# Performance work log

Hardware: AMD Instinct MI355X
Metric: run time of the kernel (lower is better)

The kernel has to match this reference:

```python
import jax, jax.numpy as jnp
import numpy as np

N = 50000      # total nodes across batched graphs
E = 400000     # directed edges (before self-loops)
B = 256        # number of graphs / protein embeddings
F_IN = 78      # atom features (num_features_xd)
H1, F1 = 10, 78   # gcn1: heads=10, out=78 -> concat 780
F2 = 128       # gcn2 output_dim (heads=1)
EMB = 320      # PLM embed_dim
PLM = 128      # plm_layers[0]
BN_EPS = 1e-5


def setup_inputs() -> dict:
    key = jax.random.key(0)
    ks = jax.random.split(key, 30)
    g = lambda k, s, sc=0.05: (jax.random.normal(k, s, jnp.float32) * sc)
    inp = {
        'x': jax.random.normal(ks[0], (N, F_IN), jnp.float32),
        'edge_index': jax.random.randint(ks[1], (2, E), 0, N),
        # deterministic sorted assignment guarantees every graph id in [0,B) is populated
        'batch': (jnp.arange(N) * B) // N,
        'target_embedding': jax.random.normal(ks[2], (B, EMB), jnp.float32),
        # GATConv 1 (78 -> 78, heads=10, concat)
        'W1': g(ks[3], (F_IN, H1 * F1)), 'a1s': g(ks[4], (H1, F1)), 'a1d': g(ks[5], (H1, F1)), 'b1': g(ks[6], (H1 * F1,)),
        # GATConv 2 (780 -> 128, heads=1)
        'W2': g(ks[7], (H1 * F1, F2)), 'a2s': g(ks[8], (1, F2)), 'a2d': g(ks[9], (1, F2)), 'b2': g(ks[10], (F2,)),
        # fc_g1
        'Wg': g(ks[11], (F2, F2)), 'bg': g(ks[12], (F2,)),
        # PLM branch: Linear(320,128) + BatchNorm1d(128) in eval mode
        'Wxt': g(ks[13], (EMB, PLM)), 'bxt': g(ks[14], (PLM,)),
        'gamma': jnp.ones((PLM,), jnp.float32), 'beta': jnp.zeros((PLM,), jnp.float32),
        'rmean': g(ks[15], (PLM,)), 'rvar': jax.random.uniform(ks[16], (PLM,), jnp.float32, 0.5, 1.5),
        # head MLP
        'Wf1': g(ks[17], (F2 + PLM, 1024)), 'bf1': g(ks[18], (1024,)),
        'Wf2': g(ks[19], (1024, 256)), 'bf2': g(ks[20], (256,)),
        'Wo': g(ks[21], (256, 1)), 'bo': g(ks[22], (1,)),
    }
    return inp


def gat_conv(x, src, dst, W, a_s, a_d, b, n):
    """PyG-style GATConv (self-loops already included in src/dst)."""
    H, F = a_s.shape
    h = (x @ W).reshape(-1, H, F)                        # [n, H, F]
    e = jax.nn.leaky_relu((h * a_s).sum(-1)[src] + (h * a_d).sum(-1)[dst], 0.2)  # [e, H]
    m = jax.ops.segment_max(e, dst, num_segments=n)      # segment softmax over incoming edges
    p = jnp.exp(e - m[dst])
    denom = jax.ops.segment_sum(p, dst, num_segments=n)
    alpha = p / denom[dst]                               # [e, H]
    out = jax.ops.segment_sum(alpha[:, :, None] * h[src], dst, num_segments=n)  # [n, H, F]
    return out.reshape(-1, H * F) + b


def reference(x, edge_index, batch, target_embedding, W1, a1s, a1d, b1, W2, a2s, a2d, b2,
              Wg, bg, Wxt, bxt, gamma, beta, rmean, rvar, Wf1, bf1, Wf2, bf2, Wo, bo):
    n = x.shape[0]
    loop = jnp.arange(n)
    src = jnp.concatenate([edge_index[0], loop])   # add self-loops (GATConv default)
    dst = jnp.concatenate([edge_index[1], loop])
    h = jax.nn.elu(gat_conv(x, src, dst, W1, a1s, a1d, b1, n))      # [N, 780]
    h = jax.nn.relu(gat_conv(h, src, dst, W2, a2s, a2d, b2, n))     # [N, 128]
    g = jax.ops.segment_max(h, batch, num_segments=B)               # global max pool [B, 128]
    g = jax.nn.relu(g @ Wg + bg)
    xt = target_embedding @ Wxt + bxt
    xt = jax.nn.relu((xt - rmean) / jnp.sqrt(rvar + BN_EPS) * gamma + beta)  # BN eval
    xc = jnp.concatenate([g, xt], axis=1)                           # [B, 256]
    xc = jax.nn.relu(xc @ Wf1 + bf1)
    xc = jax.nn.relu(xc @ Wf2 + bf2)
    return xc @ Wo + bo                                             # [B, 1]
```

## Files before the change

### kernel.cpp

```cpp
#include <hip/hip_runtime.h>
#include <hip/hip_fp16.h>
#include <math.h>

static constexpr int F2 = 128, EMB = 320;

typedef _Float16 h8v __attribute__((ext_vector_type(8)));
typedef float f4v __attribute__((ext_vector_type(4)));

union F4H2 { float4 f; __half2 h[4]; };
union F2H2 { float2 f; __half2 h[2]; };

__device__ __forceinline__ __half2 shfl_xor_h2(__half2 v, int off) {
    union { __half2 h; float f; } u;
    u.h = v;
    u.f = __shfl_xor(u.f, off);
    return u.h;
}

__device__ __forceinline__ void esd(const int* src, const int* dst, int E, int e, int& s, int& d) {
    if (e < E) { s = src[e]; d = dst[e]; }
    else       { s = e - E; d = s; }
}

__global__ void k_count(const int* __restrict__ src, const int* __restrict__ dst, int E, int Etot,
                        int* __restrict__ cnt) {
    int e = blockIdx.x * 256 + threadIdx.x;
    if (e >= Etot) return;
    int s, d;
    esd(src, dst, E, e, s, d);
    atomicAdd(&cnt[d], 1);
}

__global__ void k_scan1(const int* __restrict__ in, int* __restrict__ out, int* __restrict__ bsum,
                        int n) {
    __shared__ int tmp[256];
    int t = threadIdx.x;
    int gid = blockIdx.x * 256 + t;
    int v = gid < n ? in[gid] : 0;
    tmp[t] = v;
    __syncthreads();
    for (int off = 1; off < 256; off <<= 1) {
        int u = (t >= off) ? tmp[t - off] : 0;
        __syncthreads();
        tmp[t] += u;
        __syncthreads();
    }
    if (gid < n) out[gid] = tmp[t] - v;
    if (t == 255) bsum[blockIdx.x] = tmp[255];
}

__global__ void k_scan2(int* __restrict__ bsum, int nb) {
    __shared__ int tmp[256];
    __shared__ int carry;
    int t = threadIdx.x;
    if (t == 0) carry = 0;
    __syncthreads();
    for (int base = 0; base < nb; base += 256) {
        int i = base + t;
        int v = (i < nb) ? bsum[i] : 0;
        tmp[t] = v;
        __syncthreads();
        for (int off = 1; off < 256; off <<= 1) {
            int u = (t >= off) ? tmp[t - off] : 0;
            __syncthreads();
            tmp[t] += u;
            __syncthreads();
        }
        if (i < nb) bsum[i] = tmp[t] - v + carry;
        __syncthreads();
        if (t == 0) carry += tmp[255];
        __syncthreads();
    }
}

__global__ void k_scan3(int* __restrict__ out, const int* __restrict__ bsum, int n, int Etot,
                        int* __restrict__ rp_last, int* __restrict__ cur) {
    int gid = blockIdx.x * 256 + threadIdx.x;
    if (gid < n) {
        int v = out[gid] + bsum[blockIdx.x];
        out[gid] = v;
        cur[gid] = v;
    }
    if (gid == 0) rp_last[0] = Etot;
}

__global__ void k_scatter(const int* __restrict__ src, const int* __restrict__ dst, int E, int Etot,
                          int* __restrict__ cur, int* __restrict__ csrc) {
    int e = blockIdx.x * 256 + threadIdx.x;
    if (e >= Etot) return;
    int s, d;
    esd(src, dst, E, e, s, d);
    int pos = atomicAdd(&cur[d], 1);
    csrc[pos] = s;
}

__global__ void k_prep_w(const float* __restrict__ W1, const float* __restrict__ a1s,
                         const float* __restrict__ a1d, const float* __restrict__ W2,
                         __half* __restrict__ W1T, float* __restrict__ wes,
                         float* __restrict__ wed, __half* __restrict__ W2T) {
    int idx = blockIdx.x * 256 + threadIdx.x;
    if (idx < 76800) {
        int h = idx / (80 * 96), r = idx % (80 * 96), c = r / 96, k = r % 96;
        float v = (c < 78 && k < 78) ? W1[(size_t)k * 780 + h * 78 + c] : 0.f;
        W1T[idx] = __float2half(v);
    } else if (idx < 77600) {
        int j = idx - 76800;
        int h = j / 80, k = j % 80;
        float s = 0.f, d = 0.f;
        if (k < 78) {
            for (int f = 0; f < 78; f++) {
                float w = W1[(size_t)k * 780 + h * 78 + f];
                s = fmaf(w, a1s[h * 78 + f], s);
                d = fmaf(w, a1d[h * 78 + f], d);
            }
        }
        wes[j] = s;
        wed[j] = d;
    } else if (idx < 77600 + 102400) {
        int j = idx - 77600;
        int c = j / 800, k = j % 800;
        float v = (k < 780) ? W2[(size_t)k * 128 + c] : 0.f;
        W2T[j] = __float2half(v);
    }
}

__global__ void k_prep_xpk(const float* __restrict__ x, __half2* __restrict__ xpk, int N) {
    int idx = blockIdx.x * 256 + threadIdx.x;
    if (idx >= N * 64) return;
    int n = idx >> 6, l = idx & 63;
    float lo = x[(size_t)n * 78 + l];
    float hi = (64 + l < 78) ? x[(size_t)n * 78 + 64 + l] : 0.f;
    xpk[idx] = __floats2half2_rn(lo, hi);
}

__global__ void k_coefx(const float* __restrict__ x, const float* __restrict__ wes,
                        const float* __restrict__ wed, float* __restrict__ esg,
                        float* __restrict__ edg, int N) {
    int n = blockIdx.x * 256 + threadIdx.x;
    if (n >= N) return;
    float es[10] = {}, ed[10] = {};
    const float* xr = x + (size_t)n * 78;
    for (int k = 0; k < 78; k++) {
        float xv = xr[k];
#pragma unroll
        for (int h = 0; h < 10; h++) {
            es[h] = fmaf(xv, wes[h * 80 + k], es[h]);
            ed[h] = fmaf(xv, wed[h * 80 + k], ed[h]);
        }
    }
#pragma unroll
    for (int h = 0; h < 10; h++) {
        esg[(size_t)n * 16 + h] = es[h];
        edg[(size_t)n * 16 + h] = ed[h];
    }
}

__global__ void k_gatx10(const int* __restrict__ rp, const int* __restrict__ csrc,
                         const float* __restrict__ esg, const float* __restrict__ edg,
                         const __half2* __restrict__ xpk, __half* __restrict__ xagg, int N) {
    __shared__ __align__(16) __half2 pl[4][64][12];
    __shared__ __align__(16) int sl[4][64];
    int w = threadIdx.x >> 6, lane = threadIdx.x & 63;
    int node = blockIdx.x * 4 + w;
    if (node >= N) return;
    int beg = rp[node], end = rp[node + 1];
    int deg = end - beg;

    float edn[10];
    {
        const float* ep = edg + (size_t)node * 16;
        float4 a = *(const float4*)ep, b = *(const float4*)(ep + 4);
        float2 c = *(const float2*)(ep + 8);
        edn[0] = a.x; edn[1] = a.y; edn[2] = a.z; edn[3] = a.w;
        edn[4] = b.x; edn[5] = b.y; edn[6] = b.z; edn[7] = b.w;
        edn[8] = c.x; edn[9] = c.y;
    }

    __half2 acc[10];
#pragma unroll
    for (int h = 0; h < 10; h++) acc[h] = __floats2half2_rn(0.f, 0.f);

#define PASSC_BODY(LIMIT)                                                          \
    for (int i0 = 0; i0 < (LIMIT); i0 += 4) {                                      \
        int4 s4 = *(const int4*)&sl[w][i0];                                        \
        __half2 xr0 = xpk[(size_t)s4.x * 64 + lane];                               \
        __half2 xr1 = xpk[(size_t)s4.y * 64 + lane];                               \
        __half2 xr2 = xpk[(size_t)s4.z * 64 + lane];                               \
        __half2 xr3 = xpk[(size_t)s4.w * 64 + lane];                               \
        _Pragma("unroll")                                                          \
        for (int j = 0; j < 4; j++) {                                              \
            F4H2 qa, qb; F2H2 qc;                                                  \
            qa.f = *(const float4*)&pl[w][i0 + j][0];                              \
            qb.f = *(const float4*)&pl[w][i0 + j][4];                              \
            qc.f = *(const float2*)&pl[w][i0 + j][8];                              \
            __half2 xr = (j == 0) ? xr0 : (j == 1) ? xr1 : (j == 2) ? xr2 : xr3;   \
            acc[0] = __hfma2(qa.h[0], xr, acc[0]);                                 \
            acc[1] = __hfma2(qa.h[1], xr, acc[1]);                                 \
            acc[2] = __hfma2(qa.h[2], xr, acc[2]);                                 \
            acc[3] = __hfma2(qa.h[3], xr, acc[3]);                                 \
            acc[4] = __hfma2(qb.h[0], xr, acc[4]);                                 \
            acc[5] = __hfma2(qb.h[1], xr, acc[5]);                                 \
            acc[6] = __hfma2(qb.h[2], xr, acc[6]);                                 \
            acc[7] = __hfma2(qb.h[3], xr, acc[7]);                                 \
            acc[8] = __hfma2(qc.h[0], xr, acc[8]);                                 \
            acc[9] = __hfma2(qc.h[1], xr, acc[9]);                                 \
        }                                                                          \
    }

#define STASH(PVEC)                                                                \
    {                                                                              \
        F4H2 wa, wb; F2H2 wc;                                                      \
        _Pragma("unroll")                                                          \
        for (int h = 0; h < 4; h++) wa.h[h] = __float2half2_rn(PVEC[h]);           \
        _Pragma("unroll")                                                          \
        for (int h = 0; h < 4; h++) wb.h[h] = __float2half2_rn(PVEC[4 + h]);       \
        wc.h[0] = __float2half2_rn(PVEC[8]);                                       \
        wc.h[1] = __float2half2_rn(PVEC[9]);                                       \
        *(float4*)&pl[w][lane][0] = wa.f;                                          \
        *(float4*)&pl[w][lane][4] = wb.f;                                          \
        *(float2*)&pl[w][lane][8] = wc.f;                                          \
        sl[w][lane] = s;                                                           \
    }

    if (deg <= 64) {
        bool act = lane < deg;
        int s = act ? csrc[beg + lane] : 0;
        float p[10];
        if (act) {
            const float* sp = esg + (size_t)s * 16;
            float4 a = *(const float4*)sp, b = *(const float4*)(sp + 4);
            float2 c = *(const float2*)(sp + 8);
            float v[10];
            v[0] = a.x + edn[0]; v[1] = a.y + edn[1]; v[2] = a.z + edn[2]; v[3] = a.w + edn[3];
            v[4] = b.x + edn[4]; v[5] = b.y + edn[5]; v[6] = b.z + edn[6]; v[7] = b.w + edn[7];
            v[8] = c.x + edn[8]; v[9] = c.y + edn[9];
#pragma unroll
            for (int h = 0; h < 10; h++) {
                float vv = v[h] >= 0.f ? v[h] : 0.2f * v[h];
                p[h] = __expf(vv);
            }
        } else {
#pragma unroll
            for (int h = 0; h < 10; h++) p[h] = 0.f;
        }
        __half2 sh[5];
#pragma unroll
        for (int j = 0; j < 5; j++) sh[j] = __floats2half2_rn(p[2 * j], p[2 * j + 1]);
        int start = (deg <= 16) ? 8 : 32;
        for (int off = start; off; off >>= 1) {
#pragma unroll
            for (int j = 0; j < 5; j++) sh[j] = __hadd2(sh[j], shfl_xor_h2(sh[j], off));
        }
#pragma unroll
        for (int j = 0; j < 5; j++) {
            float2 f = __half22float2(sh[j]);
            p[2 * j] *= 1.f / f.x;
            p[2 * j + 1] *= 1.f / f.y;
        }
        STASH(p)
        PASSC_BODY(deg)
    } else {
        float ssf[10] = {};
        for (int cb = beg; cb < end; cb += 64) {
            int e = cb + lane;
            bool act = e < end;
            int si = act ? csrc[e] : 0;
            if (act) {
                const float* sp = esg + (size_t)si * 16;
#pragma unroll
                for (int h = 0; h < 10; h++) {
                    float vv = sp[h] + edn[h];
                    vv = vv >= 0.f ? vv : 0.2f * vv;
                    ssf[h] += __expf(vv);
                }
            }
        }
#pragma unroll
        for (int off = 32; off; off >>= 1) {
#pragma unroll
            for (int h = 0; h < 10; h++) ssf[h] += __shfl_xor(ssf[h], off);
        }
        float inv[10];
#pragma unroll
        for (int h = 0; h < 10; h++) inv[h] = 1.f / ssf[h];

        for (int cb = beg; cb < end; cb += 64) {
            int cnt = min(64, end - cb);
            int e = cb + lane;
            bool act = e < end;
            int s = act ? csrc[e] : 0;
            float p[10];
            if (act) {
                const float* sp = esg + (size_t)s * 16;
#pragma unroll
                for (int h = 0; h < 10; h++) {
                    float vv = sp[h] + edn[h];
                    vv = vv >= 0.f ? vv : 0.2f * vv;
                    p[h] = __expf(vv) * inv[h];
                }
            } else {
#pragma unroll
                for (int h = 0; h < 10; h++) p[h] = 0.f;
            }
            STASH(p)
            PASSC_BODY(cnt)
        }
    }
#undef PASSC_BODY
#undef STASH

    __half* op = xagg + (size_t)node * 800;
#pragma unroll
    for (int h = 0; h < 10; h++) {
        __half* hp = op + h * 80;
        hp[lane] = __low2half(acc[h]);
        if (lane < 16) hp[64 + lane] = __high2half(acc[h]);
    }
}

__global__ __launch_bounds__(128) void k_gemmQ(const __half* __restrict__ xagg,
                                               const __half* __restrict__ W1T,
                                               const float* __restrict__ b1,
                                               const __half* __restrict__ W2T,
                                               const float* __restrict__ a2s,
                                               const float* __restrict__ a2d,
                                               __half* __restrict__ h216,
                                               float* __restrict__ es2,
                                               float* __restrict__ ed2, int N) {
    constexpr int LQ = 808;
    __shared__ __align__(16) _Float16 qlds[16 * LQ];
    __shared__ float sered[2][2][16];
    int w = threadIdx.x >> 6, lane = threadIdx.x & 63;
    int row0 = blockIdx.x * 16;
    int col16 = lane & 15, grp = lane >> 4;
    int ko = grp * 8;
    int rbase = grp * 4;
    int ar = min(row0 + col16, N - 1);

    for (int i = threadIdx.x; i < 16 * 28; i += 128) {
        int r = i / 28, c = 780 + i % 28;
        qlds[r * LQ + c] = (_Float16)0.f;
    }

    const _Float16* Ab = (const _Float16*)xagg + (size_t)ar * 800 + ko;
#pragma unroll
    for (int hh = 0; hh < 5; hh++) {
        int h = w * 5 + hh;
        f4v acc1[5] = {};
        const _Float16* Ap = Ab + h * 80;
        const _Float16* Bp = (const _Float16*)W1T + ((size_t)h * 80 + col16) * 96 + ko;
#pragma unroll
        for (int ks = 0; ks < 3; ks++) {
            h8v a = *(const h8v*)(Ap + ks * 32);
#pragma unroll
            for (int t = 0; t < 5; t++) {
                h8v b = *(const h8v*)(Bp + (size_t)t * 16 * 96 + ks * 32);
                acc1[t] = __builtin_amdgcn_mfma_f32_16x16x32_f16(a, b, acc1[t], 0, 0, 0);
            }
        }
#pragma unroll
        for (int t = 0; t < 5; t++) {
            int c = t * 16 + col16;
            if (c < 78) {
                float bias = b1[h * 78 + c];
#pragma unroll
                for (int r = 0; r < 4; r++) {
                    float v = acc1[t][r] + bias;
                    float e = v > 0.f ? v : (__expf(v) - 1.f);
                    qlds[(rbase + r) * LQ + h * 78 + c] = (_Float16)e;
                }
            }
        }
    }
    __syncthreads();

    f4v acc[4] = {};
    const _Float16* Bq = (const _Float16*)W2T + (size_t)col16 * 800 + ko;
    const _Float16* Aq = qlds + (size_t)col16 * LQ + ko;
    for (int ks = 0; ks < 25; ks++) {
        h8v a = *(const h8v*)(Aq + ks * 32);
#pragma unroll
        for (int t = 0; t < 4; t++) {
            h8v b = *(const h8v*)(Bq + (size_t)(w * 4 + t) * 16 * 800 + ks * 32);
            acc[t] = __builtin_amdgcn_mfma_f32_16x16x32_f16(a, b, acc[t], 0, 0, 0);
        }
    }
    float wa[4], wb[4];
#pragma unroll
    for (int t = 0; t < 4; t++) {
        wa[t] = a2s[(w * 4 + t) * 16 + col16];
        wb[t] = a2d[(w * 4 + t) * 16 + col16];
    }
#pragma unroll
    for (int r = 0; r < 4; r++) {
        int n = row0 + rbase + r;
        float se = 0.f, sd = 0.f;
#pragma unroll
        for (int t = 0; t < 4; t++) {
            float v = acc[t][r];
            se = fmaf(v, wa[t], se);
            sd = fmaf(v, wb[t], sd);
            if (n < N) h216[(size_t)n * 128 + (w * 4 + t) * 16 + col16] = __float2half(v);
        }
#pragma unroll
        for (int off = 1; off < 16; off <<= 1) {
            se += __shfl_xor(se, off);
            sd += __shfl_xor(sd, off);
        }
        if (col16 == 0) {
            sered[w][0][rbase + r] = se;
            sered[w][1][rbase + r] = sd;
        }
    }
    __syncthreads();
    if (threadIdx.x < 16) {
        int n = row0 + threadIdx.x;
        if (n < N) {
            es2[n] = sered[0][0][threadIdx.x] + sered[1][0][threadIdx.x];
            ed2[n] = sered[0][1][threadIdx.x] + sered[1][1][threadIdx.x];
        }
    }
}

__global__ void k_gatP(const int* __restrict__ rp, const int* __restrict__ csrc,
                       const float* __restrict__ es, const float* __restrict__ ed,
                       const __half2* __restrict__ h216, const float* __restrict__ b2,
                       const int* __restrict__ batch, unsigned* __restrict__ gb, int N) {
    __shared__ float red[4][128];
    __shared__ int bids[4];
    __shared__ __align__(16) __half2 plP[4][64];
    __shared__ __align__(16) int slP[4][64];
    int w = threadIdx.x >> 6, lane = threadIdx.x & 63;
    int node = blockIdx.x * 4 + w;
    bool valid = node < N;

    __half2 acc = __floats2half2_rn(0.f, 0.f);
    int bid = -1;

#define PASSC2(LIMIT)                                                      \
    for (int i0 = 0; i0 < (LIMIT); i0 += 4) {                              \
        int4 s4 = *(const int4*)&slP[w][i0];                               \
        F4H2 q; q.f = *(const float4*)&plP[w][i0];                         \
        __half2 f0 = h216[(size_t)s4.x * 64 + lane];                       \
        __half2 f1 = h216[(size_t)s4.y * 64 + lane];                       \
        __half2 f2 = h216[(size_t)s4.z * 64 + lane];                       \
        __half2 f3 = h216[(size_t)s4.w * 64 + lane];                       \
        acc = __hfma2(q.h[0], f0, acc);                                    \
        acc = __hfma2(q.h[1], f1, acc);                                    \
        acc = __hfma2(q.h[2], f2, acc);                                    \
        acc = __hfma2(q.h[3], f3, acc);                                    \
    }

    if (valid) {
        int beg = rp[node], end = rp[node + 1];
        int deg = end - beg;
        float edn = ed[node];
        bid = batch[node];

        if (deg <= 64) {
            bool act = lane < deg;
            int s = act ? csrc[beg + lane] : 0;
            float p = 0.f;
            if (act) {
                float v = es[s] + edn;
                v = v >= 0.f ? v : 0.2f * v;
                p = __expf(v);
            }
            float ss = p;
            int start = (deg <= 16) ? 8 : 32;
            for (int off = start; off; off >>= 1) ss += __shfl_xor(ss, off);
            p *= 1.f / ss;
            plP[w][lane] = __float2half2_rn(p);
            slP[w][lane] = s;
            PASSC2(deg)
        } else {
            float ss = 0.f;
            for (int cb = beg; cb < end; cb += 64) {
                int e = cb + lane;
                bool act = e < end;
                int s = act ? csrc[e] : 0;
                if (act) {
                    float v = es[s] + edn;
                    v = v >= 0.f ? v : 0.2f * v;
                    ss += __expf(v);
                }
            }
#pragma unroll
            for (int off = 32; off; off >>= 1) ss += __shfl_xor(ss, off);
            float inv = 1.f / ss;
            for (int cb = beg; cb < end; cb += 64) {
                int cnt = min(64, end - cb);
                int e = cb + lane;
                bool act = e < end;
                int s = act ? csrc[e] : 0;
                float p = 0.f;
                if (act) {
                    float v = es[s] + edn;
                    v = v >= 0.f ? v : 0.2f * v;
                    p = __expf(v) * inv;
                }
                plP[w][lane] = __float2half2_rn(p);
                slP[w][lane] = s;
                PASSC2(cnt)
            }
        }
    }
#undef PASSC2

    float2 af = __half22float2(acc);
    red[w][2 * lane]     = valid ? fmaxf(af.x + b2[2 * lane], 0.f) : 0.f;
    red[w][2 * lane + 1] = valid ? fmaxf(af.y + b2[2 * lane + 1], 0.f) : 0.f;
    if (lane == 0) bids[w] = valid ? bid : -1;
    __syncthreads();
    if (threadIdx.x < 128) {
        int c = threadIdx.x;
        int b0 = bids[0];
        bool same = (bids[1] == b0) && (bids[2] == b0) && (bids[3] == b0);
        if (same && b0 >= 0) {
            float m = fmaxf(fmaxf(red[0][c], red[1][c]), fmaxf(red[2][c], red[3][c]));
            atomicMax(&gb[(size_t)b0 * 128 + c], __float_as_uint(m));
        } else {
#pragma unroll
            for (int w2 = 0; w2 < 4; w2++) {
                if (bids[w2] >= 0)
                    atomicMax(&gb[(size_t)bids[w2] * 128 + c], __float_as_uint(red[w2][c]));
            }
        }
    }
}

__global__ void k_head_g(const unsigned* __restrict__ gbits, const float* __restrict__ Wg,
                         const float* __restrict__ bg, float* __restrict__ xc) {
    int b = blockIdx.x, c = threadIdx.x;
    __shared__ float srow[F2];
    srow[c] = __uint_as_float(gbits[(size_t)b * F2 + c]);
    __syncthreads();
    float acc = bg[c];
    for (int k = 0; k < F2; k++) acc = fmaf(srow[k], Wg[k * F2 + c], acc);
    xc[(size_t)b * 256 + c] = fmaxf(acc, 0.f);
}

__global__ void k_head_xt(const float* __restrict__ te, const float* __restrict__ Wxt,
                          const float* __restrict__ bxt, const float* __restrict__ gamma,
                          const float* __restrict__ beta, const float* __restrict__ rmean,
                          const float* __restrict__ rvar, float* __restrict__ xc) {
    int b = blockIdx.x, c = threadIdx.x;
    __shared__ float srow[EMB];
    for (int k = c; k < EMB; k += 128) srow[k] = te[(size_t)b * EMB + k];
    __syncthreads();
    float acc = bxt[c];
    for (int k = 0; k < EMB; k++) acc = fmaf(srow[k], Wxt[k * F2 + c], acc);
    acc = (acc - rmean[c]) * rsqrtf(rvar[c] + 1e-5f) * gamma[c] + beta[c];
    xc[(size_t)b * 256 + 128 + c] = fmaxf(acc, 0.f);
}

__global__ void k_head_f1(const float* __restrict__ xc, const float* __restrict__ W,
                          const float* __restrict__ bias, float* __restrict__ o) {
    int b = blockIdx.x;
    __shared__ float srow[256];
    srow[threadIdx.x] = xc[(size_t)b * 256 + threadIdx.x];
    __syncthreads();
    for (int col = threadIdx.x; col < 1024; col += 256) {
        float acc = bias[col];
        for (int k = 0; k < 256; k++) acc = fmaf(srow[k], W[k * 1024 + col], acc);
        o[(size_t)b * 1024 + col] = fmaxf(acc, 0.f);
    }
}

__global__ void k_head_f2(const float* __restrict__ in, const float* __restrict__ W,
                          const float* __restrict__ bias, float* __restrict__ o) {
    int b = blockIdx.x;
    int col = threadIdx.x;
    __shared__ float srow[1024];
    for (int k = col; k < 1024; k += 256) srow[k] = in[(size_t)b * 1024 + k];
    __syncthreads();
    float acc = bias[col];
    for (int k = 0; k < 1024; k++) acc = fmaf(srow[k], W[k * 256 + col], acc);
    o[(size_t)b * 256 + col] = fmaxf(acc, 0.f);
}

__global__ void k_head_out(const float* __restrict__ in, const float* __restrict__ Wo,
                           const float* __restrict__ bo, float* __restrict__ out) {
    int b = blockIdx.x;
    float acc = 0.f;
    for (int k = threadIdx.x; k < 256; k += 64) acc = fmaf(in[(size_t)b * 256 + k], Wo[k], acc);
    for (int off = 32; off; off >>= 1) acc += __shfl_down(acc, off);
    if (threadIdx.x == 0) out[b] = acc + bo[0];
}

extern "C" void kernel_launch(void* const* d_in, const int* in_sizes, int n_in,
                              void* d_out, int out_size, void* d_ws, size_t ws_size,
                              hipStream_t stream) {
    const float* x     = (const float*)d_in[0];
    const int*   ei    = (const int*)d_in[1];
    const int*   batch = (const int*)d_in[2];
    const float* te    = (const float*)d_in[3];
    const float* W1    = (const float*)d_in[4];
    const float* a1s   = (const float*)d_in[5];
    const float* a1d   = (const float*)d_in[6];
    const float* b1    = (const float*)d_in[7];
    const float* W2    = (const float*)d_in[8];
    const float* a2s   = (const float*)d_in[9];
    const float* a2d   = (const float*)d_in[10];
    const float* b2    = (const float*)d_in[11];
    const float* Wg    = (const float*)d_in[12];
    const float* bg    = (const float*)d_in[13];
    const float* Wxt   = (const float*)d_in[14];
    const float* bxt   = (const float*)d_in[15];
    const float* gamma = (const float*)d_in[16];
    const float* beta  = (const float*)d_in[17];
    const float* rmean = (const float*)d_in[18];
    const float* rvar  = (const float*)d_in[19];
    const float* Wf1   = (const float*)d_in[20];
    const float* bf1   = (const float*)d_in[21];
    const float* Wf2   = (const float*)d_in[22];
    const float* bf2   = (const float*)d_in[23];
    const float* Wo    = (const float*)d_in[24];
    const float* bo    = (const float*)d_in[25];

    const int N = in_sizes[0] / 78;
    const int E = in_sizes[1] / 2;
    const int B = in_sizes[3] / EMB;
    const int Etot = E + N;
    const int* src = ei;
    const int* dst = ei + E;

    char* p = (char*)d_ws;
    auto alloc = [&](size_t bytes) -> void* {
        void* r = p;
        p += (bytes + 255) & ~(size_t)255;
        return r;
    };
    __half2*  xpk  = (__half2*)alloc((size_t)N * 64 * 4);
    __half*   xagg = (__half*)alloc((size_t)N * 800 * 2 + 256);
    __half*   h216 = (__half*)alloc((size_t)N * 128 * 2);
    float*    esg  = (float*)alloc((size_t)N * 16 * 4);
    float*    edg  = (float*)alloc((size_t)N * 16 * 4);
    float*    es2  = (float*)alloc((size_t)N * 4);
    float*    ed2  = (float*)alloc((size_t)N * 4);
    __half*   W1T  = (__half*)alloc((size_t)10 * 80 * 96 * 2);
    __half*   W2T  = (__half*)alloc((size_t)128 * 800 * 2);
    float*    wes  = (float*)alloc((size_t)800 * 4);
    float*    wed  = (float*)alloc((size_t)800 * 4);
    int*      cnt  = (int*)alloc((size_t)N * 4);
    int*      rp   = (int*)alloc((size_t)(N + 1) * 4);
    int*      cur  = (int*)alloc((size_t)N * 4);
    int*      csrc = (int*)alloc((size_t)Etot * 4);
    int*      bsum = (int*)alloc((size_t)1024 * 4);
    unsigned* gb   = (unsigned*)alloc((size_t)B * F2 * 4);
    float*    xc   = (float*)alloc((size_t)B * 256 * 4);
    float*    f1o  = (float*)alloc((size_t)B * 1024 * 4);
    float*    f2o  = (float*)alloc((size_t)B * 256 * 4);

    auto gsz = [](long long t) { return (int)((t + 255) / 256); };
    const int nb = gsz(N);
    const int nwave = (N + 3) / 4;
    const int nrow16 = (N + 15) / 16;

    hipMemsetAsync(cnt, 0, (size_t)N * 4, stream);
    k_count<<<gsz(Etot), 256, 0, stream>>>(src, dst, E, Etot, cnt);
    k_scan1<<<nb, 256, 0, stream>>>(cnt, rp, bsum, N);
    k_scan2<<<1, 256, 0, stream>>>(bsum, nb);
    k_scan3<<<nb, 256, 0, stream>>>(rp, bsum, N, Etot, rp + N, cur);
    k_scatter<<<gsz(Etot), 256, 0, stream>>>(src, dst, E, Etot, cur, csrc);

    k_prep_w<<<gsz(180000), 256, 0, stream>>>(W1, a1s, a1d, W2, W1T, wes, wed, W2T);
    k_prep_xpk<<<gsz((long long)N * 64), 256, 0, stream>>>(x, xpk, N);
    k_coefx<<<nb, 256, 0, stream>>>(x, wes, wed, esg, edg, N);
    hipMemsetAsync(gb, 0, (size_t)B * F2 * 4, stream);

    k_gatx10<<<nwave, 256, 0, stream>>>(rp, csrc, esg, edg, xpk, xagg, N);

    k_gemmQ<<<nrow16, 128, 0, stream>>>(xagg, W1T, b1, W2T, a2s, a2d, h216, es2, ed2, N);

    k_gatP<<<nwave, 256, 0, stream>>>(rp, csrc, es2, ed2, (const __half2*)h216, b2, batch, gb, N);

    k_head_g<<<B, 128, 0, stream>>>(gb, Wg, bg, xc);
    k_head_xt<<<B, 128, 0, stream>>>(te, Wxt, bxt, gamma, beta, rmean, rvar, xc);
    k_head_f1<<<B, 256, 0, stream>>>(xc, Wf1, bf1, f1o);
    k_head_f2<<<B, 256, 0, stream>>>(f1o, Wf2, bf2, f2o);
    k_head_out<<<B, 64, 0, stream>>>(f2o, Wo, bo, (float*)d_out);
}
```

Before: 339.5 us.

## Interleave GEMM1 head chunks with GEMM2 in k_gemmQ to shrink LDS

The fused GEMM kernel now processes the 10 GAT heads in 5 chunks of two heads. Each chunk's ELU output goes into a small LDS tile and is immediately consumed by the second GEMM, instead of staging the full 16x780 activation row in LDS first. W2 is re-laid out per head with 96-column padding so the K-slices line up with the chunk layout. This cuts LDS from about 26KB to about 6KB per block to raise occupancy. The cost is two barriers per chunk and extra padded MFMA work (960 vs 800 K).

Result: slower. 376.9 us (+11.0%).

```diff
diff --git a/kernel.cpp b/kernel.cpp
--- a/kernel.cpp
+++ b/kernel.cpp
@@ -97,7 +97,7 @@
 __global__ void k_prep_w(const float* __restrict__ W1, const float* __restrict__ a1s,
                          const float* __restrict__ a1d, const float* __restrict__ W2,
                          __half* __restrict__ W1T, float* __restrict__ wes,
-                         float* __restrict__ wed, __half* __restrict__ W2T) {
+                         float* __restrict__ wed, __half* __restrict__ W2Tq) {
     int idx = blockIdx.x * 256 + threadIdx.x;
     if (idx < 76800) {
         int h = idx / (80 * 96), r = idx % (80 * 96), c = r / 96, k = r % 96;
@@ -116,11 +116,11 @@
         }
         wes[j] = s;
         wed[j] = d;
-    } else if (idx < 77600 + 102400) {
+    } else if (idx < 77600 + 128 * 960) {
         int j = idx - 77600;
-        int c = j / 800, k = j % 800;
-        float v = (k < 780) ? W2[(size_t)k * 128 + c] : 0.f;
-        W2T[j] = __float2half(v);
+        int c = j / 960, r = j % 960, h = r / 96, k = r % 96;
+        float v = (k < 78) ? W2[(size_t)(h * 78 + k) * 128 + c] : 0.f;
+        W2Tq[j] = __float2half(v);
     }
 }
 
@@ -321,13 +321,13 @@
 __global__ __launch_bounds__(128) void k_gemmQ(const __half* __restrict__ xagg,
                                                const __half* __restrict__ W1T,
                                                const float* __restrict__ b1,
-                                               const __half* __restrict__ W2T,
+                                               const __half* __restrict__ W2Tq,
                                                const float* __restrict__ a2s,
                                                const float* __restrict__ a2d,
                                                __half* __restrict__ h216,
                                                float* __restrict__ es2,
                                                float* __restrict__ ed2, int N) {
-    constexpr int LQ = 808;
+    constexpr int LQ = 200;
     __shared__ __align__(16) _Float16 qlds[16 * LQ];
     __shared__ float sered[2][2][16];
     int w = threadIdx.x >> 6, lane = threadIdx.x & 63;
@@ -337,15 +337,16 @@
     int rbase = grp * 4;
     int ar = min(row0 + col16, N - 1);
 
-    for (int i = threadIdx.x; i < 16 * 28; i += 128) {
-        int r = i / 28, c = 780 + i % 28;
-        qlds[r * LQ + c] = (_Float16)0.f;
+    for (int i = threadIdx.x; i < 16 * LQ / 8; i += 128) {
+        ((float4*)qlds)[i] = float4{0.f, 0.f, 0.f, 0.f};
     }
 
     const _Float16* Ab = (const _Float16*)xagg + (size_t)ar * 800 + ko;
-#pragma unroll
-    for (int hh = 0; hh < 5; hh++) {
-        int h = w * 5 + hh;
+    f4v acc[4] = {};
+
+#pragma unroll
+    for (int ch = 0; ch < 5; ch++) {
+        int h = 2 * ch + w;
         f4v acc1[5] = {};
         const _Float16* Ap = Ab + h * 80;
         const _Float16* Bp = (const _Float16*)W1T + ((size_t)h * 80 + col16) * 96 + ko;
@@ -367,24 +368,26 @@
                 for (int r = 0; r < 4; r++) {
                     float v = acc1[t][r] + bias;
                     float e = v > 0.f ? v : (__expf(v) - 1.f);
-                    qlds[(rbase + r) * LQ + h * 78 + c] = (_Float16)e;
+                    qlds[(rbase + r) * LQ + w * 96 + c] = (_Float16)e;
                 }
             }
         }
-    }
-    __syncthreads();
-
-    f4v acc[4] = {};
-    const _Float16* Bq = (const _Float16*)W2T + (size_t)col16 * 800 + ko;
-    const _Float16* Aq = qlds + (size_t)col16 * LQ + ko;
-    for (int ks = 0; ks < 25; ks++) {
-        h8v a = *(const h8v*)(Aq + ks * 32);
-#pragma unroll
-        for (int t = 0; t < 4; t++) {
-            h8v b = *(const h8v*)(Bq + (size_t)(w * 4 + t) * 16 * 800 + ks * 32);
-            acc[t] = __builtin_amdgcn_mfma_f32_16x16x32_f16(a, b, acc[t], 0, 0, 0);
-        }
-    }
+        __syncthreads();
+        const _Float16* Aq = qlds + (size_t)col16 * LQ + ko;
+        const _Float16* Bq = (const _Float16*)W2Tq + (size_t)((w * 4) * 16 + col16) * 960 +
+                             ch * 192 + ko;
+#pragma unroll
+        for (int ks = 0; ks < 6; ks++) {
+            h8v a = *(const h8v*)(Aq + ks * 32);
+#pragma unroll
+            for (int t = 0; t < 4; t++) {
+                h8v b = *(const h8v*)(Bq + (size_t)t * 16 * 960 + ks * 32);
+                acc[t] = __builtin_amdgcn_mfma_f32_16x16x32_f16(a, b, acc[t], 0, 0, 0);
+            }
+        }
+        __syncthreads();
+    }
+
     float wa[4], wb[4];
 #pragma unroll
     for (int t = 0; t < 4; t++) {
@@ -639,7 +642,7 @@
     float*    es2  = (float*)alloc((size_t)N * 4);
     float*    ed2  = (float*)alloc((size_t)N * 4);
     __half*   W1T  = (__half*)alloc((size_t)10 * 80 * 96 * 2);
-    __half*   W2T  = (__half*)alloc((size_t)128 * 800 * 2);
+    __half*   W2Tq = (__half*)alloc((size_t)128 * 960 * 2);
     float*    wes  = (float*)alloc((size_t)800 * 4);
     float*    wed  = (float*)alloc((size_t)800 * 4);
     int*      cnt  = (int*)alloc((size_t)N * 4);
@@ -664,14 +667,14 @@
     k_scan3<<<nb, 256, 0, stream>>>(rp, bsum, N, Etot, rp + N, cur);
     k_scatter<<<gsz(Etot), 256, 0, stream>>>(src, dst, E, Etot, cur, csrc);
 
-    k_prep_w<<<gsz(180000), 256, 0, stream>>>(W1, a1s, a1d, W2, W1T, wes, wed, W2T);
+    k_prep_w<<<gsz(77600 + 128 * 960), 256, 0, stream>>>(W1, a1s, a1d, W2, W1T, wes, wed, W2Tq);
     k_prep_xpk<<<gsz((long long)N * 64), 256, 0, stream>>>(x, xpk, N);
     k_coefx<<<nb, 256, 0, stream>>>(x, wes, wed, esg, edg, N);
     hipMemsetAsync(gb, 0, (size_t)B * F2 * 4, stream);
 
     k_gatx10<<<nwave, 256, 0, stream>>>(rp, csrc, esg, edg, xpk, xagg, N);
 
-    k_gemmQ<<<nrow16, 128, 0, stream>>>(xagg, W1T, b1, W2T, a2s, a2d, h216, es2, ed2, N);
+    k_gemmQ<<<nrow16, 128, 0, stream>>>(xagg, W1T, b1, W2Tq, a2s, a2d, h216, es2, ed2, N);
 
     k_gatP<<<nwave, 256, 0, stream>>>(rp, csrc, es2, ed2, (const __half2*)h216, b2, batch, gb, N);
 
```
